# Kernel tuning notes

Hardware: AMD Instinct MI355X
Metric: run time of the kernel (lower is better)

The kernel has to match this reference:

```python
import jax, jax.numpy as jnp
import numpy as np

N_QUBITS = 12
N_LAYERS = 1
DIM = 1 << N_QUBITS
SUB_DIM = 1 << (N_QUBITS // 2)
# use_wscale=True, lrmul=1, gain=sqrt(2): init_std=1, w_mul = gain*5**-0.5
W_MUL = (2.0 ** 0.5) * (5.0 ** -0.5)


def _cnot_perm(n_qubits, n_layers):
    """Composite permutation of all CNOT gates (each CNOT permutes basis states).

    Applying gates g1..gk in sequence to a state v gives v_out[j] = v[p1(p2(...pk(j)))]
    (each CNOT perm is an involution). qubit 0 = most significant bit.
    """
    dim = 1 << n_qubits
    gates = []
    for _ in range(n_layers):
        for q in range(n_qubits - 1):
            gates.append((q, q + 1))
        gates.append((n_qubits - 1, 0))
    perm = np.arange(dim)
    for (c, t) in reversed(gates):
        bc = n_qubits - 1 - c
        bt = n_qubits - 1 - t
        perm = perm ^ (((perm >> bc) & 1) << bt)
    return perm

CNOT_PERM = _cnot_perm(N_QUBITS, N_LAYERS)


def _xyz_layer_unitary(w):
    """Kron of per-qubit Rz(w_z) @ Ry(w_y) @ Rx(w_x); w shape (3n,) float."""
    n = N_QUBITS
    tx, ty, tz = w[:n], w[n:2 * n], w[2 * n:3 * n]
    cx, sx = jnp.cos(tx / 2), jnp.sin(tx / 2)
    zero = jnp.zeros_like(cx)
    Rx = jnp.stack([jnp.stack([cx + 0j, -1j * sx], -1),
                    jnp.stack([-1j * sx, cx + 0j], -1)], -2)        # (n,2,2)
    cy, sy = jnp.cos(ty / 2), jnp.sin(ty / 2)
    Ry = jnp.stack([jnp.stack([cy + 0j, -sy + 0j], -1),
                    jnp.stack([sy + 0j, cy + 0j], -1)], -2)
    ez = jnp.exp(-1j * tz / 2)
    Rz = jnp.stack([jnp.stack([ez, zero + 0j], -1),
                    jnp.stack([zero + 0j, jnp.conj(ez)], -1)], -2)
    G = jnp.einsum('qab,qbc,qcd->qad', Rz, Ry, Rx)                  # (n,2,2)
    U = G[0]
    for q in range(1, n):
        U = jnp.kron(U, G[q])
    return U.astype(jnp.complex64)                                   # (DIM,DIM)


def _circuit_unitary(weight):
    w = (weight * W_MUL)[:3 * N_QUBITS]
    L = _xyz_layer_unitary(w)
    # U = L2 @ C @ L1 with L2 == L1 == L; C@L1 is a row gather by the CNOT perm
    return L @ L[CNOT_PERM, :]


def _evolve_and_ptrace(U, A, B, dA, dB):
    bsz = A.shape[0]
    # batched kron -> [B, DIM, DIM] complex density matrix
    rho = jnp.einsum('bij,bkl->bikjl', A, B).reshape(bsz, DIM, DIM).astype(jnp.complex64)
    out = U @ rho @ U.conj().T                                       # [B,DIM,DIM]
    out = out.reshape(bsz, dA, dB, dA, dB)
    return jnp.einsum('bikjk->bij', out)                             # Tr_B -> [B,dA,dA]


def setup_inputs() -> dict:
    key = jax.random.key(0)
    kA, kB, kW = jax.random.split(key, 3)
    inputA = jax.random.normal(kA, (2, SUB_DIM, SUB_DIM), dtype=jnp.float32)
    inputB = jax.random.normal(kB, (2, SUB_DIM, SUB_DIM), dtype=jnp.float32)
    weight = jax.random.uniform(kW, (6 * N_QUBITS,), dtype=jnp.float32) * (2 * np.pi)
    return {"inputA": inputA, "inputB": inputB, "weight": weight,
            "dimA": SUB_DIM, "dimB": SUB_DIM}


def reference(inputA, inputB, weight, dimA, dimB):
    assert dimA == dimB
    U = _circuit_unitary(weight)
    mutualBatA = _evolve_and_ptrace(U, inputA, inputB, dimA, dimB)
    mutualAatB = _evolve_and_ptrace(U, inputB, inputA, dimA, dimB)
    return (mutualBatA, mutualAatB)
```

## Files before the change

### kernel.cpp

```cpp
#include <hip/hip_runtime.h>
#include <hip/hip_bf16.h>


#define W_MUL 0.6324555320336759f

__device__ __forceinline__ float2 cmul(float2 a, float2 b) {
    return make_float2(a.x * b.x - a.y * b.y, a.x * b.y + a.y * b.x);
}
__device__ __forceinline__ float2 cadd(float2 a, float2 b) { return make_float2(a.x + b.x, a.y + b.y); }
__device__ __forceinline__ float2 csub(float2 a, float2 b) { return make_float2(a.x - b.x, a.y - b.y); }
__device__ __forceinline__ float2 conjc(float2 a) { return make_float2(a.x, -a.y); }
__device__ __forceinline__ float2 cfma(float2 a, float2 b, float2 c) {
    c.x = fmaf(a.x, b.x, fmaf(-a.y, b.y, c.x));
    c.y = fmaf(a.x, b.y, fmaf( a.y, b.x, c.y));
    return c;
}
__device__ __forceinline__ float2 cfmac(float2 a, float2 b, float2 c) {
    c.x = fmaf(a.x, b.x, fmaf( a.y, b.y, c.x));
    c.y = fmaf(a.x, b.y, fmaf(-a.y, b.x, c.y));
    return c;
}

__device__ __forceinline__ void make_G(const float* w, int q, float2 G[2][2]) {
    float tx = w[q]      * (W_MUL * 0.5f);
    float ty = w[12 + q] * (W_MUL * 0.5f);
    float tz = w[24 + q] * (W_MUL * 0.5f);
    float cx, sx, cy, sy, cz, sz;
    sincosf(tx, &sx, &cx);
    sincosf(ty, &sy, &cy);
    sincosf(tz, &sz, &cz);
    float2 M00 = make_float2( cy * cx,  sy * sx);
    float2 M01 = make_float2(-sy * cx, -cy * sx);
    float2 M10 = make_float2( sy * cx, -cy * sx);
    float2 M11 = make_float2( cy * cx, -sy * sx);
    float2 ez  = make_float2(cz, -sz);
    float2 ezc = make_float2(cz,  sz);
    G[0][0] = cmul(ez,  M00);
    G[0][1] = cmul(ez,  M01);
    G[1][0] = cmul(ezc, M10);
    G[1][1] = cmul(ezc, M11);
}

__device__ __forceinline__ void build_LH(const float2 G[6][2][2], float2* dst, int t, int nt) {
    for (int e = t; e < 4096; e += nt) {
        int i = e >> 6, j = e & 63;
        float2 p = G[0][(i >> 5) & 1][(j >> 5) & 1];
        p = cmul(p, G[1][(i >> 4) & 1][(j >> 4) & 1]);
        p = cmul(p, G[2][(i >> 3) & 1][(j >> 3) & 1]);
        p = cmul(p, G[3][(i >> 2) & 1][(j >> 2) & 1]);
        p = cmul(p, G[4][(i >> 1) & 1][(j >> 1) & 1]);
        p = cmul(p, G[5][(i     ) & 1][(j     ) & 1]);
        dst[j * 64 + i] = conjc(p);
    }
}

__device__ __forceinline__ void make_tables(const float2 G[6][2][2],
                                            float2 zt[6][2][2], float2 x6[2][2], float2 xz6[2][2]) {
    #pragma unroll
    for (int q = 0; q < 6; ++q)
        #pragma unroll
        for (int a = 0; a < 2; ++a)
            #pragma unroll
            for (int b = 0; b < 2; ++b) {
                float2 g0a = G[q][0][a], g0b = G[q][0][b];
                float2 g1a = G[q][1][a], g1b = G[q][1][b];
                zt[q][a][b] = csub(cmul(conjc(g0a), g0b), cmul(conjc(g1a), g1b));
                if (q == 0) {
                    x6[a][b]  = cadd(cmul(conjc(g0a), g1b), cmul(conjc(g1a), g0b));
                    xz6[a][b] = csub(cmul(conjc(g1a), g0b), cmul(conjc(g0a), g1b));
                }
            }
}

__device__ __forceinline__ void trace_acc(const float* Xr, const float2 zt[6][2][2],
                                          const float2 x6[2][2], const float2 xz6[2][2],
                                          int t, int nt, float acc[7]) {
    for (int e = t; e < 4096; e += nt) {
        int r = e >> 6, c = e & 63;
        float xv = Xr[e];
        float2 P = zt[1][(c >> 4) & 1][(r >> 4) & 1];
        P = cmul(P, zt[2][(c >> 3) & 1][(r >> 3) & 1]);
        P = cmul(P, zt[3][(c >> 2) & 1][(r >> 2) & 1]);
        P = cmul(P, zt[4][(c >> 1) & 1][(r >> 1) & 1]);
        P = cmul(P, zt[5][c & 1][r & 1]);
        float2 pz  = cmul(zt[0][c >> 5][r >> 5], P);
        float2 pxz = cmul(xz6[c >> 5][r >> 5], P);
        acc[0] = fmaf(pz.x,  xv, acc[0]); acc[1] = fmaf(pz.y,  xv, acc[1]);
        acc[2] = fmaf(pxz.x, xv, acc[2]); acc[3] = fmaf(pxz.y, xv, acc[3]);
        if ((c & 31) == (r & 31)) {
            float2 kx = x6[c >> 5][r >> 5];
            acc[4] = fmaf(kx.x, xv, acc[4]); acc[5] = fmaf(kx.y, xv, acc[5]);
            if (c == r) acc[6] += xv;
        }
    }
}

template <int NT>
__device__ __forceinline__ bool reduce7(float acc[7], float (*red)[8], int t) {
    #pragma unroll
    for (int o = 32; o; o >>= 1)
        #pragma unroll
        for (int m = 0; m < 7; ++m) acc[m] += __shfl_down(acc[m], o);
    if ((t & 63) == 0)
        for (int m = 0; m < 7; ++m) red[t >> 6][m] = acc[m];
    __syncthreads();
    if (t == 0) {
        for (int m = 0; m < 7; ++m) {
            float s = 0.f;
            for (int wv = 0; wv < NT / 64; ++wv) s += red[wv][m];
            acc[m] = s;
        }
        return true;
    }
    return false;
}

__device__ __forceinline__ void pick_cc(int p, int q, float2 e0, float2 e1, float2 f0, float2 f1,
                                        float2& c0, float2& c1) {
    if (p & 1) { if (q & 1) { c0 = e1; c1 = e0; } else { c0 = f1; c1 = f0; } }
    else       { if (q & 1) { c0 = f0; c1 = f1; } else { c0 = e0; c1 = e1; } }
}

template <int OM>
__device__ __forceinline__ void write_out(void* outv, int ev, int i, int tc, float2 r0, float2 r1) {
    if constexpr (OM == 0) {
        float* og = (float*)outv + (ev << 12) + (i << 6);
        og[tc] = r0.x; og[tc + 32] = r1.x;
    } else if constexpr (OM == 1) {
        __hip_bfloat16* og = (__hip_bfloat16*)outv + (ev << 13) + (i << 7);
        og[2 * tc]      = __float2bfloat16(r0.x); og[2 * tc + 1]  = __float2bfloat16(r0.y);
        og[2 * tc + 64] = __float2bfloat16(r1.x); og[2 * tc + 65] = __float2bfloat16(r1.y);
    } else {
        float2* og = (float2*)outv + (ev << 12) + (i << 6);
        og[tc] = r0; og[tc + 32] = r1;
    }
}

__global__ __launch_bounds__(512) void qk1(const float* __restrict__ A, const float* __restrict__ B,
                                           const float* __restrict__ w, float2* __restrict__ ws) {
    __shared__ float2 LAH[4096];
    __shared__ float  Xr[4096];
    __shared__ float2 TMP[1024];
    __shared__ float2 G6[6][2][2];
    __shared__ float  red[8][8];

    const int bx = blockIdx.x;
    const int t  = threadIdx.x;

    if (bx < 16) {
        const int x  = bx >> 2;
        const int I0 = (bx & 3) << 4;
        const float* Xg = (x < 2) ? (A + x * 4096) : (B + (x - 2) * 4096);
        if (t < 6) make_G(w, t, G6[t]);
        __syncthreads();
        build_LH(G6, LAH, t, 512);
        for (int e = t; e < 4096; e += 512) Xr[e] = Xg[e];
        __syncthreads();

        const int tr = t >> 5, tc = t & 31;
        const int i  = I0 + tr;
        float2 a0 = make_float2(0, 0), a1 = make_float2(0, 0);
        #pragma unroll 16
        for (int k = 0; k < 64; ++k) {
            float2 la = LAH[(k << 6) + i];
            float x0 = Xr[(k << 6) + tc], x1 = Xr[(k << 6) + tc + 32];
            a0.x = fmaf(la.x, x0, a0.x); a0.y = fmaf(-la.y, x0, a0.y);
            a1.x = fmaf(la.x, x1, a1.x); a1.y = fmaf(-la.y, x1, a1.y);
        }
        TMP[(tr << 6) + tc] = a0; TMP[(tr << 6) + tc + 32] = a1;
        __syncthreads();
        float2 c0 = make_float2(0, 0), c1 = make_float2(0, 0);
        #pragma unroll 16
        for (int k = 0; k < 64; ++k) {
            float2 tm = TMP[(tr << 6) + k];
            float2 l0 = LAH[(k << 6) + tc], l1 = LAH[(k << 6) + tc + 32];
            c0 = cfma(tm, l0, c0); c1 = cfma(tm, l1, c1);
        }
        ws[(x << 12) + (i << 6) + tc]      = c0;
        ws[(x << 12) + (i << 6) + tc + 32] = c1;
    } else {
        const int x = bx - 16;
        const float* Xg = (x < 2) ? (A + x * 4096) : (B + (x - 2) * 4096);
        if (t < 6) make_G(w, 6 + t, G6[t]);
        for (int e = t; e < 4096; e += 512) Xr[e] = Xg[e];
        __syncthreads();
        float2 zt[6][2][2], x6[2][2], xz6[2][2];
        make_tables(G6, zt, x6, xz6);
        float acc[7] = {0, 0, 0, 0, 0, 0, 0};
        trace_acc(Xr, zt, x6, xz6, t, 512, acc);
        if (reduce7<512>(acc, red, t)) {
            float2* S = ws + 16384 + (x << 2);
            S[0] = make_float2(0.5f * (acc[6] + acc[0]),  0.5f * acc[1]);
            S[1] = make_float2(0.5f * (acc[6] - acc[0]), -0.5f * acc[1]);
            S[2] = make_float2(0.5f * (acc[4] + acc[2]),  0.5f * (acc[5] + acc[3]));
            S[3] = make_float2(0.5f * (acc[4] - acc[2]),  0.5f * (acc[5] - acc[3]));
        }
    }
}

template <int OM>
__global__ __launch_bounds__(512) void qk2(const float* __restrict__ w, const float2* __restrict__ ws,
                                           void* __restrict__ outv) {
    __shared__ float2 LAH[4096];
    __shared__ float2 A1s[4096];
    __shared__ float2 Ts[4096];
    __shared__ float2 Us[1024];
    __shared__ float2 G6[6][2][2];

    const int bx = blockIdx.x;
    const int ev = bx >> 2, rq = bx & 3;
    const int order = ev >> 1, b = ev & 1;
    const int x1 = order ? 2 + b : b;
    const int x2 = order ? b : 2 + b;
    const int t = threadIdx.x;

    if (t < 6) make_G(w, t, G6[t]);
    __syncthreads();
    build_LH(G6, LAH, t, 512);
    for (int e = t; e < 4096; e += 512) A1s[e] = ws[(x1 << 12) + e];
    __syncthreads();

    const float2 e0 = ws[16384 + (x2 << 2) + 0];
    const float2 e1 = ws[16384 + (x2 << 2) + 1];
    const float2 f0 = ws[16384 + (x2 << 2) + 2];
    const float2 f1 = ws[16384 + (x2 << 2) + 3];

    for (int idx = t; idx < 4096; idx += 512) {
        int p = idx >> 6, q = idx & 63;
        int u = p ^ (p >> 1), v = q ^ (q >> 1);
        float2 c0, c1;
        pick_cc(p, q, e0, e1, f0, f1, c0, c1);
        float2 a  = A1s[(u << 6) + v];
        float2 a2 = A1s[((u ^ 48) << 6) + (v ^ 48)];
        Ts[idx] = cadd(cmul(a, c0), cmul(a2, c1));
    }
    __syncthreads();

    const int tr = t >> 5, tc = t & 31;
    const int i = (rq << 4) + tr;
    float2 u0 = make_float2(0, 0), u1 = make_float2(0, 0);
    #pragma unroll 16
    for (int k = 0; k < 64; ++k) {
        float2 la = LAH[(k << 6) + i];
        u0 = cfmac(la, Ts[(k << 6) + tc], u0);
        u1 = cfmac(la, Ts[(k << 6) + tc + 32], u1);
    }
    Us[(tr << 6) + tc] = u0; Us[(tr << 6) + tc + 32] = u1;
    __syncthreads();
    float2 r0 = make_float2(0, 0), r1 = make_float2(0, 0);
    #pragma unroll 16
    for (int k = 0; k < 64; ++k) {
        float2 uu = Us[(tr << 6) + k];
        r0 = cfma(uu, LAH[(k << 6) + tc], r0);
        r1 = cfma(uu, LAH[(k << 6) + tc + 32], r1);
    }
    write_out<OM>(outv, ev, i, tc, r0, r1);
}

template <int OM>
__global__ __launch_bounds__(1024) void qmono(const float* __restrict__ A, const float* __restrict__ B,
                                              const float* __restrict__ w, void* __restrict__ outv) {
    __shared__ float2 LAH[4096];
    __shared__ float  Xr[4096];
    __shared__ float2 BA[4096];
    __shared__ float2 BB[4096];
    __shared__ float2 G6[6][2][2];
    __shared__ float  red[16][8];
    __shared__ float2 Sq[4];

    const int ev = blockIdx.x;
    const int order = ev >> 1, b = ev & 1;
    const int t = threadIdx.x;
    const float* X1g = (order ? B : A) + b * 4096;
    const float* X2g = (order ? A : B) + b * 4096;

    if (t < 6) make_G(w, t, G6[t]);
    __syncthreads();
    build_LH(G6, LAH, t, 1024);
    for (int e = t; e < 4096; e += 1024) Xr[e] = X1g[e];
    __syncthreads();

    const int tr = t >> 5, tc = t & 31;
    const int i0 = tr, i1 = tr + 32;
    {
        float2 a00 = {0,0}, a01 = {0,0}, a10 = {0,0}, a11 = {0,0};
        #pragma unroll 16
        for (int k = 0; k < 64; ++k) {
            float2 la0 = LAH[(k << 6) + i0], la1 = LAH[(k << 6) + i1];
            float x0 = Xr[(k << 6) + tc], x1 = Xr[(k << 6) + tc + 32];
            a00.x = fmaf(la0.x, x0, a00.x); a00.y = fmaf(-la0.y, x0, a00.y);
            a01.x = fmaf(la0.x, x1, a01.x); a01.y = fmaf(-la0.y, x1, a01.y);
            a10.x = fmaf(la1.x, x0, a10.x); a10.y = fmaf(-la1.y, x0, a10.y);
            a11.x = fmaf(la1.x, x1, a11.x); a11.y = fmaf(-la1.y, x1, a11.y);
        }
        BA[(i0 << 6) + tc] = a00; BA[(i0 << 6) + tc + 32] = a01;
        BA[(i1 << 6) + tc] = a10; BA[(i1 << 6) + tc + 32] = a11;
    }
    __syncthreads();
    {
        float2 a00 = {0,0}, a01 = {0,0}, a10 = {0,0}, a11 = {0,0};
        #pragma unroll 16
        for (int k = 0; k < 64; ++k) {
            float2 t0 = BA[(i0 << 6) + k], t1 = BA[(i1 << 6) + k];
            float2 l0 = LAH[(k << 6) + tc], l1 = LAH[(k << 6) + tc + 32];
            a00 = cfma(t0, l0, a00); a01 = cfma(t0, l1, a01);
            a10 = cfma(t1, l0, a10); a11 = cfma(t1, l1, a11);
        }
        BB[(i0 << 6) + tc] = a00; BB[(i0 << 6) + tc + 32] = a01;
        BB[(i1 << 6) + tc] = a10; BB[(i1 << 6) + tc + 32] = a11;
    }
    __syncthreads();
    for (int e = t; e < 4096; e += 1024) Xr[e] = X2g[e];
    if (t < 6) make_G(w, 6 + t, G6[t]);
    __syncthreads();
    {
        float2 zt[6][2][2], x6[2][2], xz6[2][2];
        make_tables(G6, zt, x6, xz6);
        float acc[7] = {0, 0, 0, 0, 0, 0, 0};
        trace_acc(Xr, zt, x6, xz6, t, 1024, acc);
        if (reduce7<1024>(acc, red, t)) {
            Sq[0] = make_float2(0.5f * (acc[6] + acc[0]),  0.5f * acc[1]);
            Sq[1] = make_float2(0.5f * (acc[6] - acc[0]), -0.5f * acc[1]);
            Sq[2] = make_float2(0.5f * (acc[4] + acc[2]),  0.5f * (acc[5] + acc[3]));
            Sq[3] = make_float2(0.5f * (acc[4] - acc[2]),  0.5f * (acc[5] - acc[3]));
        }
    }
    __syncthreads();
    const float2 e0 = Sq[0], e1 = Sq[1], f0 = Sq[2], f1 = Sq[3];
    for (int idx = t; idx < 4096; idx += 1024) {
        int p = idx >> 6, q = idx & 63;
        int u = p ^ (p >> 1), v = q ^ (q >> 1);
        float2 c0, c1;
        pick_cc(p, q, e0, e1, f0, f1, c0, c1);
        float2 a  = BB[(u << 6) + v];
        float2 a2 = BB[((u ^ 48) << 6) + (v ^ 48)];
        BA[idx] = cadd(cmul(a, c0), cmul(a2, c1));
    }
    __syncthreads();
    {
        float2 a00 = {0,0}, a01 = {0,0}, a10 = {0,0}, a11 = {0,0};
        #pragma unroll 16
        for (int k = 0; k < 64; ++k) {
            float2 la0 = LAH[(k << 6) + i0], la1 = LAH[(k << 6) + i1];
            float2 t0 = BA[(k << 6) + tc], t1 = BA[(k << 6) + tc + 32];
            a00 = cfmac(la0, t0, a00); a01 = cfmac(la0, t1, a01);
            a10 = cfmac(la1, t0, a10); a11 = cfmac(la1, t1, a11);
        }
        __syncthreads();
        BB[(i0 << 6) + tc] = a00; BB[(i0 << 6) + tc + 32] = a01;
        BB[(i1 << 6) + tc] = a10; BB[(i1 << 6) + tc + 32] = a11;
    }
    __syncthreads();
    {
        float2 a00 = {0,0}, a01 = {0,0}, a10 = {0,0}, a11 = {0,0};
        #pragma unroll 16
        for (int k = 0; k < 64; ++k) {
            float2 u0 = BB[(i0 << 6) + k], u1 = BB[(i1 << 6) + k];
            float2 l0 = LAH[(k << 6) + tc], l1 = LAH[(k << 6) + tc + 32];
            a00 = cfma(u0, l0, a00); a01 = cfma(u0, l1, a01);
            a10 = cfma(u1, l0, a10); a11 = cfma(u1, l1, a11);
        }
        write_out<OM>(outv, ev, i0, tc, a00, a01);
        write_out<OM>(outv, ev, i1, tc, a10, a11);
    }
}

extern "C" void kernel_launch(void* const* d_in, const int* in_sizes, int n_in,
                              void* d_out, int out_size, void* d_ws, size_t ws_size,
                              hipStream_t stream) {
    const float* A = (const float*)d_in[0];
    const float* B = (const float*)d_in[1];
    const float* w = (const float*)d_in[2];
    (void)in_sizes; (void)n_in;
    const bool two = (ws_size >= 16400u * sizeof(float2));
    if (two) {
        qk1<<<20, 512, 0, stream>>>(A, B, w, (float2*)d_ws);
        if (out_size == 16384)      qk2<0><<<16, 512, 0, stream>>>(w, (const float2*)d_ws, d_out);
        else if (out_size == 32768) qk2<1><<<16, 512, 0, stream>>>(w, (const float2*)d_ws, d_out);
        else                        qk2<2><<<16, 512, 0, stream>>>(w, (const float2*)d_ws, d_out);
    } else {
        if (out_size == 16384)      qmono<0><<<4, 1024, 0, stream>>>(A, B, w, d_out);
        else if (out_size == 32768) qmono<1><<<4, 1024, 0, stream>>>(A, B, w, d_out);
        else                        qmono<2><<<4, 1024, 0, stream>>>(A, B, w, d_out);
    }
}
```

Baseline: 81.69 us.

## Fuse two-kernel pipeline into one kernel with redundant per-block recompute

Replaces the two-launch path (qk1 writing to workspace, then qk2) with a single fused kernel that launches 16 blocks of 1024 threads. Each block redundantly recomputes the full first-stage products and trace for its evolution, then computes only a quarter of the output rows in the final two matmuls. This removes one kernel launch and the round-trip through global workspace. In exchange every block repeats the first-stage work, so total work grows fourfold for that stage.

```diff
diff --git a/kernel.cpp b/kernel.cpp
--- a/kernel.cpp
+++ b/kernel.cpp
@@ -122,144 +122,8 @@
 }
 
 template <int OM>
-__device__ __forceinline__ void write_out(void* outv, int ev, int i, int tc, float2 r0, float2 r1) {
-    if constexpr (OM == 0) {
-        float* og = (float*)outv + (ev << 12) + (i << 6);
-        og[tc] = r0.x; og[tc + 32] = r1.x;
-    } else if constexpr (OM == 1) {
-        __hip_bfloat16* og = (__hip_bfloat16*)outv + (ev << 13) + (i << 7);
-        og[2 * tc]      = __float2bfloat16(r0.x); og[2 * tc + 1]  = __float2bfloat16(r0.y);
-        og[2 * tc + 64] = __float2bfloat16(r1.x); og[2 * tc + 65] = __float2bfloat16(r1.y);
-    } else {
-        float2* og = (float2*)outv + (ev << 12) + (i << 6);
-        og[tc] = r0; og[tc + 32] = r1;
-    }
-}
-
-__global__ __launch_bounds__(512) void qk1(const float* __restrict__ A, const float* __restrict__ B,
-                                           const float* __restrict__ w, float2* __restrict__ ws) {
-    __shared__ float2 LAH[4096];
-    __shared__ float  Xr[4096];
-    __shared__ float2 TMP[1024];
-    __shared__ float2 G6[6][2][2];
-    __shared__ float  red[8][8];
-
-    const int bx = blockIdx.x;
-    const int t  = threadIdx.x;
-
-    if (bx < 16) {
-        const int x  = bx >> 2;
-        const int I0 = (bx & 3) << 4;
-        const float* Xg = (x < 2) ? (A + x * 4096) : (B + (x - 2) * 4096);
-        if (t < 6) make_G(w, t, G6[t]);
-        __syncthreads();
-        build_LH(G6, LAH, t, 512);
-        for (int e = t; e < 4096; e += 512) Xr[e] = Xg[e];
-        __syncthreads();
-
-        const int tr = t >> 5, tc = t & 31;
-        const int i  = I0 + tr;
-        float2 a0 = make_float2(0, 0), a1 = make_float2(0, 0);
-        #pragma unroll 16
-        for (int k = 0; k < 64; ++k) {
-            float2 la = LAH[(k << 6) + i];
-            float x0 = Xr[(k << 6) + tc], x1 = Xr[(k << 6) + tc + 32];
-            a0.x = fmaf(la.x, x0, a0.x); a0.y = fmaf(-la.y, x0, a0.y);
-            a1.x = fmaf(la.x, x1, a1.x); a1.y = fmaf(-la.y, x1, a1.y);
-        }
-        TMP[(tr << 6) + tc] = a0; TMP[(tr << 6) + tc + 32] = a1;
-        __syncthreads();
-        float2 c0 = make_float2(0, 0), c1 = make_float2(0, 0);
-        #pragma unroll 16
-        for (int k = 0; k < 64; ++k) {
-            float2 tm = TMP[(tr << 6) + k];
-            float2 l0 = LAH[(k << 6) + tc], l1 = LAH[(k << 6) + tc + 32];
-            c0 = cfma(tm, l0, c0); c1 = cfma(tm, l1, c1);
-        }
-        ws[(x << 12) + (i << 6) + tc]      = c0;
-        ws[(x << 12) + (i << 6) + tc + 32] = c1;
-    } else {
-        const int x = bx - 16;
-        const float* Xg = (x < 2) ? (A + x * 4096) : (B + (x - 2) * 4096);
-        if (t < 6) make_G(w, 6 + t, G6[t]);
-        for (int e = t; e < 4096; e += 512) Xr[e] = Xg[e];
-        __syncthreads();
-        float2 zt[6][2][2], x6[2][2], xz6[2][2];
-        make_tables(G6, zt, x6, xz6);
-        float acc[7] = {0, 0, 0, 0, 0, 0, 0};
-        trace_acc(Xr, zt, x6, xz6, t, 512, acc);
-        if (reduce7<512>(acc, red, t)) {
-            float2* S = ws + 16384 + (x << 2);
-            S[0] = make_float2(0.5f * (acc[6] + acc[0]),  0.5f * acc[1]);
-            S[1] = make_float2(0.5f * (acc[6] - acc[0]), -0.5f * acc[1]);
-            S[2] = make_float2(0.5f * (acc[4] + acc[2]),  0.5f * (acc[5] + acc[3]));
-            S[3] = make_float2(0.5f * (acc[4] - acc[2]),  0.5f * (acc[5] - acc[3]));
-        }
-    }
-}
-
-template <int OM>
-__global__ __launch_bounds__(512) void qk2(const float* __restrict__ w, const float2* __restrict__ ws,
-                                           void* __restrict__ outv) {
-    __shared__ float2 LAH[4096];
-    __shared__ float2 A1s[4096];
-    __shared__ float2 Ts[4096];
-    __shared__ float2 Us[1024];
-    __shared__ float2 G6[6][2][2];
-
-    const int bx = blockIdx.x;
-    const int ev = bx >> 2, rq = bx & 3;
-    const int order = ev >> 1, b = ev & 1;
-    const int x1 = order ? 2 + b : b;
-    const int x2 = order ? b : 2 + b;
-    const int t = threadIdx.x;
-
-    if (t < 6) make_G(w, t, G6[t]);
-    __syncthreads();
-    build_LH(G6, LAH, t, 512);
-    for (int e = t; e < 4096; e += 512) A1s[e] = ws[(x1 << 12) + e];
-    __syncthreads();
-
-    const float2 e0 = ws[16384 + (x2 << 2) + 0];
-    const float2 e1 = ws[16384 + (x2 << 2) + 1];
-    const float2 f0 = ws[16384 + (x2 << 2) + 2];
-    const float2 f1 = ws[16384 + (x2 << 2) + 3];
-
-    for (int idx = t; idx < 4096; idx += 512) {
-        int p = idx >> 6, q = idx & 63;
-        int u = p ^ (p >> 1), v = q ^ (q >> 1);
-        float2 c0, c1;
-        pick_cc(p, q, e0, e1, f0, f1, c0, c1);
-        float2 a  = A1s[(u << 6) + v];
-        float2 a2 = A1s[((u ^ 48) << 6) + (v ^ 48)];
-        Ts[idx] = cadd(cmul(a, c0), cmul(a2, c1));
-    }
-    __syncthreads();
-
-    const int tr = t >> 5, tc = t & 31;
-    const int i = (rq << 4) + tr;
-    float2 u0 = make_float2(0, 0), u1 = make_float2(0, 0);
-    #pragma unroll 16
-    for (int k = 0; k < 64; ++k) {
-        float2 la = LAH[(k << 6) + i];
-        u0 = cfmac(la, Ts[(k << 6) + tc], u0);
-        u1 = cfmac(la, Ts[(k << 6) + tc + 32], u1);
-    }
-    Us[(tr << 6) + tc] = u0; Us[(tr << 6) + tc + 32] = u1;
-    __syncthreads();
-    float2 r0 = make_float2(0, 0), r1 = make_float2(0, 0);
-    #pragma unroll 16
-    for (int k = 0; k < 64; ++k) {
-        float2 uu = Us[(tr << 6) + k];
-        r0 = cfma(uu, LAH[(k << 6) + tc], r0);
-        r1 = cfma(uu, LAH[(k << 6) + tc + 32], r1);
-    }
-    write_out<OM>(outv, ev, i, tc, r0, r1);
-}
-
-template <int OM>
-__global__ __launch_bounds__(1024) void qmono(const float* __restrict__ A, const float* __restrict__ B,
-                                              const float* __restrict__ w, void* __restrict__ outv) {
+__global__ __launch_bounds__(1024) void qfused(const float* __restrict__ A, const float* __restrict__ B,
+                                               const float* __restrict__ w, void* __restrict__ outv) {
     __shared__ float2 LAH[4096];
     __shared__ float  Xr[4096];
     __shared__ float2 BA[4096];
@@ -268,7 +132,8 @@
     __shared__ float  red[16][8];
     __shared__ float2 Sq[4];
 
-    const int ev = blockIdx.x;
+    const int bx = blockIdx.x;
+    const int ev = bx >> 2, rq = bx & 3;
     const int order = ev >> 1, b = ev & 1;
     const int t = threadIdx.x;
     const float* X1g = (order ? B : A) + b * 4096;
@@ -282,6 +147,7 @@
 
     const int tr = t >> 5, tc = t & 31;
     const int i0 = tr, i1 = tr + 32;
+
     {
         float2 a00 = {0,0}, a01 = {0,0}, a10 = {0,0}, a11 = {0,0};
         #pragma unroll 16
@@ -297,6 +163,7 @@
         BA[(i1 << 6) + tc] = a10; BA[(i1 << 6) + tc + 32] = a11;
     }
     __syncthreads();
+
     {
         float2 a00 = {0,0}, a01 = {0,0}, a10 = {0,0}, a11 = {0,0};
         #pragma unroll 16
@@ -310,6 +177,7 @@
         BB[(i1 << 6) + tc] = a10; BB[(i1 << 6) + tc + 32] = a11;
     }
     __syncthreads();
+
     for (int e = t; e < 4096; e += 1024) Xr[e] = X2g[e];
     if (t < 6) make_G(w, 6 + t, G6[t]);
     __syncthreads();
@@ -326,42 +194,48 @@
         }
     }
     __syncthreads();
-    const float2 e0 = Sq[0], e1 = Sq[1], f0 = Sq[2], f1 = Sq[3];
-    for (int idx = t; idx < 4096; idx += 1024) {
-        int p = idx >> 6, q = idx & 63;
-        int u = p ^ (p >> 1), v = q ^ (q >> 1);
-        float2 c0, c1;
-        pick_cc(p, q, e0, e1, f0, f1, c0, c1);
-        float2 a  = BB[(u << 6) + v];
-        float2 a2 = BB[((u ^ 48) << 6) + (v ^ 48)];
-        BA[idx] = cadd(cmul(a, c0), cmul(a2, c1));
-    }
-    __syncthreads();
-    {
-        float2 a00 = {0,0}, a01 = {0,0}, a10 = {0,0}, a11 = {0,0};
-        #pragma unroll 16
-        for (int k = 0; k < 64; ++k) {
-            float2 la0 = LAH[(k << 6) + i0], la1 = LAH[(k << 6) + i1];
-            float2 t0 = BA[(k << 6) + tc], t1 = BA[(k << 6) + tc + 32];
-            a00 = cfmac(la0, t0, a00); a01 = cfmac(la0, t1, a01);
-            a10 = cfmac(la1, t0, a10); a11 = cfmac(la1, t1, a11);
-        }
+
+    {
+        const float2 e0 = Sq[0], e1 = Sq[1], f0 = Sq[2], f1 = Sq[3];
+        for (int idx = t; idx < 4096; idx += 1024) {
+            int p = idx >> 6, q = idx & 63;
+            int u = p ^ (p >> 1), v = q ^ (q >> 1);
+            float2 c0, c1;
+            pick_cc(p, q, e0, e1, f0, f1, c0, c1);
+            float2 a  = BB[(u << 6) + v];
+            float2 a2 = BB[((u ^ 48) << 6) + (v ^ 48)];
+            BA[idx] = cadd(cmul(a, c0), cmul(a2, c1));
+        }
+    }
+    __syncthreads();
+
+    const int il = t >> 6;
+    const int i  = (rq << 4) + il;
+    const int j  = t & 63;
+    {
+        float2 u = make_float2(0, 0);
+        #pragma unroll 16
+        for (int k = 0; k < 64; ++k)
+            u = cfmac(LAH[(k << 6) + i], BA[(k << 6) + j], u);
         __syncthreads();
-        BB[(i0 << 6) + tc] = a00; BB[(i0 << 6) + tc + 32] = a01;
-        BB[(i1 << 6) + tc] = a10; BB[(i1 << 6) + tc + 32] = a11;
-    }
-    __syncthreads();
-    {
-        float2 a00 = {0,0}, a01 = {0,0}, a10 = {0,0}, a11 = {0,0};
-        #pragma unroll 16
-        for (int k = 0; k < 64; ++k) {
-            float2 u0 = BB[(i0 << 6) + k], u1 = BB[(i1 << 6) + k];
-            float2 l0 = LAH[(k << 6) + tc], l1 = LAH[(k << 6) + tc + 32];
-            a00 = cfma(u0, l0, a00); a01 = cfma(u0, l1, a01);
-            a10 = cfma(u1, l0, a10); a11 = cfma(u1, l1, a11);
-        }
-        write_out<OM>(outv, ev, i0, tc, a00, a01);
-        write_out<OM>(outv, ev, i1, tc, a10, a11);
+        BB[(il << 6) + j] = u;
+    }
+    __syncthreads();
+
+    {
+        float2 r = make_float2(0, 0);
+        #pragma unroll 16
+        for (int k = 0; k < 64; ++k)
+            r = cfma(BB[(il << 6) + k], LAH[(k << 6) + j], r);
+        if constexpr (OM == 0) {
+            ((float*)outv)[(ev << 12) + (i << 6) + j] = r.x;
+        } else if constexpr (OM == 1) {
+            __hip_bfloat16* og = (__hip_bfloat16*)outv + (ev << 13) + (i << 7);
+            og[2 * j]     = __float2bfloat16(r.x);
+            og[2 * j + 1] = __float2bfloat16(r.y);
+        } else {
+            ((float2*)outv)[(ev << 12) + (i << 6) + j] = r;
+        }
     }
 }
 
@@ -371,16 +245,8 @@
     const float* A = (const float*)d_in[0];
     const float* B = (const float*)d_in[1];
     const float* w = (const float*)d_in[2];
-    (void)in_sizes; (void)n_in;
-    const bool two = (ws_size >= 16400u * sizeof(float2));
-    if (two) {
-        qk1<<<20, 512, 0, stream>>>(A, B, w, (float2*)d_ws);
-        if (out_size == 16384)      qk2<0><<<16, 512, 0, stream>>>(w, (const float2*)d_ws, d_out);
-        else if (out_size == 32768) qk2<1><<<16, 512, 0, stream>>>(w, (const float2*)d_ws, d_out);
-        else                        qk2<2><<<16, 512, 0, stream>>>(w, (const float2*)d_ws, d_out);
-    } else {
-        if (out_size == 16384)      qmono<0><<<4, 1024, 0, stream>>>(A, B, w, d_out);
-        else if (out_size == 32768) qmono<1><<<4, 1024, 0, stream>>>(A, B, w, d_out);
-        else                        qmono<2><<<4, 1024, 0, stream>>>(A, B, w, d_out);
-    }
-}
+    (void)in_sizes; (void)n_in; (void)d_ws; (void)ws_size;
+    if (out_size == 16384)      qfused<0><<<16, 1024, 0, stream>>>(A, B, w, d_out);
+    else if (out_size == 32768) qfused<1><<<16, 1024, 0, stream>>>(A, B, w, d_out);
+    else                        qfused<2><<<16, 1024, 0, stream>>>(A, B, w, d_out);
+}
```

New measurement: 98.64 us. +20.8%, slower.
